# Kernel tuning notes

Measured on AMD Instinct MI355X. Metric: run time of the kernel, lower is better.

Reference implementation:

```python
import jax, jax.numpy as jnp
import numpy as np

B, T, N, F = 8, 64, 512, 64
H, FOUT = 128, 64
K = 3          # cheb_k
S = 3          # num_scales
EPS = 1e-8
SPARSITY = 0.3
TEMP = 1.0     # cheb_temp (buffer, temperature == 1.0)


def _xavier(key, fan_out, fan_in, gain):
    limit = gain * np.sqrt(6.0 / (fan_in + fan_out))
    return jax.random.uniform(key, (fan_out, fan_in), jnp.float32, -limit, limit)


def setup_inputs() -> dict:
    key = jax.random.key(0)
    ks = jax.random.split(key, 4)
    x = jax.random.normal(ks[0], (B, T, N, F), jnp.float32)
    # A_param: eye + 0.01*noise, symmetrized (improved_init, N > 64)
    A_param = jnp.eye(N, dtype=jnp.float32) + 0.01 * jax.random.normal(ks[1], (N, N), jnp.float32)
    A_param = 0.5 * (A_param + A_param.T)
    return {
        "x": x,
        "A_param": A_param,
        "alpha_logit": jnp.array(0.0, jnp.float32),  # logit(0.5)
        "in_w": _xavier(ks[2], H, F, np.sqrt(2.0)),
        "in_b": jnp.zeros((H,), jnp.float32),
        "out_w": _xavier(ks[3], FOUT, H, 1.0),
        "out_b": jnp.zeros((FOUT,), jnp.float32),
        "gn_in_w": jnp.ones((F,), jnp.float32), "gn_in_b": jnp.zeros((F,), jnp.float32), "gn_in_ms": jnp.ones((1,), jnp.float32),
        "gn_h_w": jnp.ones((H,), jnp.float32), "gn_h_b": jnp.zeros((H,), jnp.float32), "gn_h_ms": jnp.ones((1,), jnp.float32),
        "gn_out_w": jnp.ones((FOUT,), jnp.float32), "gn_out_b": jnp.zeros((FOUT,), jnp.float32), "gn_out_ms": jnp.ones((1,), jnp.float32),
        "cheb_w": jnp.full((S, K), 1.0 / K, jnp.float32),
        "scale_weights": jnp.full((S,), 1.0 / S, jnp.float32),
    }


def graph_norm(x, w, b, ms, eps=EPS):
    # normalize across the node dim (-2), with learnable mean scale
    mean = x.mean(axis=-2, keepdims=True)
    var = x.var(axis=-2, keepdims=True)  # biased, matches unbiased=False
    xn = (x - mean * ms) * jax.lax.rsqrt(var + eps)
    return xn * w + b


def reference(x, A_param, alpha_logit, in_w, in_b, out_w, out_b,
              gn_in_w, gn_in_b, gn_in_ms, gn_h_w, gn_h_b, gn_h_ms,
              gn_out_w, gn_out_b, gn_out_ms, cheb_w, scale_weights):
    Nv = A_param.shape[0]
    # --- learned graph (training path: tanh + adaptive top-k sparsify) ---
    A = 0.5 * (A_param + A_param.T)
    A = jnp.tanh(A / TEMP)
    k = max(1, int(Nv * (1.0 - SPARSITY)))
    _, idx = jax.lax.top_k(A, k)                       # [N, k] per-row top-k
    mask = jnp.zeros_like(A).at[jnp.arange(Nv)[:, None], idx].set(1.0)
    A_learned = A * mask
    # --- data graph (detached cosine similarity averaged over B*T) ---
    Bv, Tv, Nn, Fv = x.shape
    xt = x.reshape(Bv * Tv, Nn, Fv)
    xt = xt - xt.mean(axis=-1, keepdims=True)
    nrm = jnp.maximum(jnp.linalg.norm(xt, axis=-1, keepdims=True), EPS)
    xn = xt / nrm
    sim = jnp.einsum('bnf,bmf->bnm', xn, xn)
    A_data = jax.lax.stop_gradient(jnp.clip(sim.mean(axis=0), -1.0, 1.0))
    # --- blend ---
    alpha = jax.nn.sigmoid(alpha_logit)
    A_mix = alpha * A_learned + (1.0 - alpha) * A_data
    # --- normalized laplacian, clamped ---
    eye = jnp.eye(Nv, dtype=A_mix.dtype)
    A0 = A_mix * (1.0 - eye)
    deg = A0.sum(axis=-1)
    dinv = jnp.maximum(deg, EPS) ** -0.5
    L = jnp.clip(eye - dinv[:, None] * A0 * dinv[None, :], -1.5, 1.5)
    # --- feature pipeline ---
    xin = graph_norm(x, gn_in_w, gn_in_b, gn_in_ms)
    h = jnp.einsum('btnf,hf->btnh', xin, in_w) + in_b
    # --- multi-scale Chebyshev filter ---
    outs = []
    for s in range(S):
        if s == 0:
            L_s = L
        else:
            Lp = L
            for _ in range(s):
                Lp = Lp @ L
            L_s = jnp.clip(Lp, -1.5, 1.5)
        w = jax.nn.softmax(cheb_w[s] / TEMP)
        T0 = h
        T1 = jnp.einsum('btnf,nm->btmf', h, L_s)
        out = w[0] * T0 + w[1] * T1
        for ki in range(2, K):
            Tk = jnp.clip(2.0 * jnp.einsum('btpf,pm->btmf', T1, L_s) - T0, -50.0, 50.0)
            out = out + w[ki] * Tk
            T0, T1 = T1, Tk
        outs.append(out)
    sw = jax.nn.softmax(scale_weights)
    hc = sum(wv * o for wv, o in zip(sw, outs))
    hh = jax.nn.gelu(graph_norm(hc, gn_h_w, gn_h_b, gn_h_ms))
    y = jnp.einsum('btnh,oh->btno', hh, out_w) + out_b
    return graph_norm(y, gn_out_w, gn_out_b, gn_out_ms)
```

## Files before the change

kernel.cpp:

```cpp
#include <hip/hip_runtime.h>
#include <stdint.h>


typedef unsigned short u16;
using bf16x8 = __attribute__((ext_vector_type(8))) __bf16;
using f32x4  = __attribute__((ext_vector_type(4))) float;

#define DEV __device__ __forceinline__

DEV u16 f2b(float f) {
  union { float f; unsigned u; } v; v.f = f;
  unsigned r = v.u + 0x7FFFu + ((v.u >> 16) & 1u);
  return (u16)(r >> 16);
}
DEV float b2f(u16 b) {
  union { unsigned u; float f; } v; v.u = ((unsigned)b) << 16;
  return v.f;
}
DEV float clampf(float v, float lo, float hi) { return fminf(fmaxf(v, lo), hi); }
DEV bf16x8 pack8(const float* v) {
  union { bf16x8 b; u16 s[8]; } u;
#pragma unroll
  for (int i = 0; i < 8; ++i) u.s[i] = f2b(v[i]);
  return u.b;
}

__global__ __launch_bounds__(256) void k_fill(float* __restrict__ out, float v) {
  out[(size_t)blockIdx.x * 256 + threadIdx.x] = v;
}
__global__ __launch_bounds__(256) void k_zero(float* __restrict__ p) {
  p[(size_t)blockIdx.x * 256 + threadIdx.x] = 0.f;
}

__global__ __launch_bounds__(256) void k_Alearned(const float* __restrict__ Ap,
                                                  float* __restrict__ Aw,
                                                  const float* __restrict__ alpha_l,
                                                  const float* __restrict__ cheb_w,
                                                  const float* __restrict__ scale_w,
                                                  float* __restrict__ scal) {
  int i = blockIdx.x;
  __shared__ float row[512];
  for (int j = threadIdx.x; j < 512; j += 256)
    row[j] = tanhf(0.5f * (Ap[i * 512 + j] + Ap[j * 512 + i]));
  __syncthreads();
  for (int j = threadIdx.x; j < 512; j += 256) {
    float v = row[j];
    int rank = 0;
    for (int l = 0; l < 512; ++l) {
      float u = row[l];
      rank += (u > v) || (u == v && l < j);
    }
    Aw[i * 512 + j] = (rank < 358) ? v : 0.f;
  }
  if (i == 0 && threadIdx.x == 0) {
    float alpha = 1.f / (1.f + expf(-alpha_l[0]));
    float sm = fmaxf(fmaxf(scale_w[0], scale_w[1]), scale_w[2]);
    float e0 = expf(scale_w[0] - sm), e1 = expf(scale_w[1] - sm), e2 = expf(scale_w[2] - sm);
    float es = e0 + e1 + e2;
    float sw[3] = { e0 / es, e1 / es, e2 / es };
    float c0 = 0.f;
    for (int s = 0; s < 3; ++s) {
      float a = cheb_w[s * 3 + 0], b = cheb_w[s * 3 + 1], c = cheb_w[s * 3 + 2];
      float m = fmaxf(fmaxf(a, b), c);
      float f0 = expf(a - m), f1 = expf(b - m), f2 = expf(c - m);
      float fs = f0 + f1 + f2;
      c0 += sw[s] * (f0 / fs);
      scal[2 + s] = sw[s] * (f1 / fs);
      scal[5 + s] = sw[s] * (f2 / fs);
    }
    scal[0] = alpha;
    scal[1] = c0;
    scal[8] = c0 - (sw[0] * 0.f);
    float g = c0;
    for (int s = 0; s < 3; ++s) {
      float a = cheb_w[s * 3 + 0], b = cheb_w[s * 3 + 1], c = cheb_w[s * 3 + 2];
      float m = fmaxf(fmaxf(a, b), c);
      float f0 = expf(a - m), f1 = expf(b - m), f2 = expf(c - m);
      float fs = f0 + f1 + f2;
      g -= sw[s] * (f2 / fs);
    }
    scal[8] = g;
  }
}

__global__ __launch_bounds__(256) void k_gn_in_stats(const float* __restrict__ x,
                                                     float* __restrict__ st) {
  int bt = blockIdx.x;
  int f = threadIdx.x & 63, seg = threadIdx.x >> 6;
  float s = 0.f, s2 = 0.f;
  for (int n = seg * 128; n < seg * 128 + 128; ++n) {
    float v = x[((size_t)bt * 512 + n) * 64 + f];
    s += v; s2 += v * v;
  }
  __shared__ float ls[4][64], ls2[4][64];
  ls[seg][f] = s; ls2[seg][f] = s2;
  __syncthreads();
  if (seg == 0) {
    float ts = ls[0][f] + ls[1][f] + ls[2][f] + ls[3][f];
    float ts2 = ls2[0][f] + ls2[1][f] + ls2[2][f] + ls2[3][f];
    float mean = ts * (1.f / 512.f);
    float var = fmaxf(ts2 * (1.f / 512.f) - mean * mean, 0.f);
    st[bt * 128 + f * 2] = mean;
    st[bt * 128 + f * 2 + 1] = rsqrtf(var + 1e-8f);
  }
}

__global__ __launch_bounds__(256) void k_xn(const float* __restrict__ x,
                                            u16* __restrict__ Xt) {
  int R = blockIdx.x * 4 + (threadIdx.x >> 6);
  int lane = threadIdx.x & 63;
  int bt = R >> 9, n = R & 511;
  float v = x[(size_t)R * 64 + lane];
  float s = v;
  for (int m = 32; m; m >>= 1) s += __shfl_xor(s, m);
  float c = v - s * (1.f / 64.f);
  float q = c * c;
  for (int m = 32; m; m >>= 1) q += __shfl_xor(q, m);
  float nrm = fmaxf(sqrtf(q), 1e-8f);
  Xt[(size_t)n * 32768 + bt * 64 + lane] = f2b(c / nrm);
}

__global__ __launch_bounds__(256) void k_h(const float* __restrict__ x,
                                           const float* __restrict__ st,
                                           const float* __restrict__ gw,
                                           const float* __restrict__ gb,
                                           const float* __restrict__ msp,
                                           const float* __restrict__ in_w,
                                           const float* __restrict__ in_b,
                                           u16* __restrict__ Hmat) {
  int bt = blockIdx.x >> 1, half = blockIdx.x & 1;
  __shared__ float sc[64], sh[64], bias[128];
  int tid = threadIdx.x;
  float ms = msp[0];
  if (tid < 64) {
    float m = st[bt * 128 + tid * 2], ri = st[bt * 128 + tid * 2 + 1];
    float s = ri * gw[tid];
    sc[tid] = s;
    sh[tid] = gb[tid] - m * ms * s;
  }
  if (tid < 128) bias[tid] = in_b[tid];
  __syncthreads();
  const int lane = tid & 63, w = tid >> 6;
  const int fr = lane & 15, fg = lane >> 4;
  bf16x8 bfrag[8][2];
#pragma unroll
  for (int ni = 0; ni < 8; ++ni)
#pragma unroll
    for (int ks = 0; ks < 2; ++ks) {
      const float* p = in_w + (ni * 16 + fr) * 64 + ks * 32 + fg * 8;
      float4 v0 = *(const float4*)p, v1 = *(const float4*)(p + 4);
      float tmp[8] = { v0.x, v0.y, v0.z, v0.w, v1.x, v1.y, v1.z, v1.w };
      bfrag[ni][ks] = pack8(tmp);
    }
#pragma unroll 1
  for (int mi = 0; mi < 4; ++mi) {
    int n0 = half * 256 + w * 64 + mi * 16;
    bf16x8 af[2];
#pragma unroll
    for (int ks = 0; ks < 2; ++ks) {
      const float* p = x + ((size_t)bt * 512 + n0 + fr) * 64 + ks * 32 + fg * 8;
      float4 v0 = *(const float4*)p, v1 = *(const float4*)(p + 4);
      float raw[8] = { v0.x, v0.y, v0.z, v0.w, v1.x, v1.y, v1.z, v1.w };
      float tmp[8];
#pragma unroll
      for (int j = 0; j < 8; ++j) {
        int f = ks * 32 + fg * 8 + j;
        tmp[j] = raw[j] * sc[f] + sh[f];
      }
      af[ks] = pack8(tmp);
    }
    f32x4 a4[8] = {};
#pragma unroll
    for (int ni = 0; ni < 8; ++ni) {
      a4[ni] = __builtin_amdgcn_mfma_f32_16x16x32_bf16(af[0], bfrag[ni][0], a4[ni], 0, 0, 0);
      a4[ni] = __builtin_amdgcn_mfma_f32_16x16x32_bf16(af[1], bfrag[ni][1], a4[ni], 0, 0, 0);
    }
#pragma unroll
    for (int ni = 0; ni < 8; ++ni) {
      int col = ni * 16 + fr;
      float bi = bias[col];
      union { uint2 u; u16 s[4]; } pk;
#pragma unroll
      for (int r = 0; r < 4; ++r) pk.s[r] = f2b(a4[ni][r] + bi);
      *(uint2*)&Hmat[((size_t)bt * 128 + col) * 512 + n0 + fg * 4] = pk.u;
    }
  }
}

__global__ __launch_bounds__(256) void k_simgemm(const u16* __restrict__ Xt,
                                                 float* __restrict__ Aacc) {
  int tm = (blockIdx.x >> 2) * 128, tn = (blockIdx.x & 3) * 128;
  int kc = blockIdx.y * 2048;
  __shared__ u16 As[128][40], Bs[128][40];
  int tid = threadIdx.x;
  int lane = tid & 63, wave = tid >> 6;
  int wm = (wave >> 1) * 64, wn = (wave & 1) * 64;
  f32x4 accf[4][4] = {};
  const int fr = lane & 15, fk = (lane >> 4) * 8;
  for (int k0 = kc; k0 < kc + 2048; k0 += 32) {
#pragma unroll
    for (int g = 0; g < 2; ++g) {
      int ee = (tid + g * 256) * 8;
      int r = ee >> 5, kk = ee & 31;
      *(uint4*)&As[r][kk] = *(const uint4*)(Xt + (size_t)(tm + r) * 32768 + k0 + kk);
      *(uint4*)&Bs[r][kk] = *(const uint4*)(Xt + (size_t)(tn + r) * 32768 + k0 + kk);
    }
    __syncthreads();
    bf16x8 af[4], bfr[4];
#pragma unroll
    for (int mi = 0; mi < 4; ++mi) af[mi] = *(const bf16x8*)&As[wm + mi * 16 + fr][fk];
#pragma unroll
    for (int ni = 0; ni < 4; ++ni) bfr[ni] = *(const bf16x8*)&Bs[wn + ni * 16 + fr][fk];
#pragma unroll
    for (int mi = 0; mi < 4; ++mi)
#pragma unroll
      for (int ni = 0; ni < 4; ++ni)
        accf[mi][ni] = __builtin_amdgcn_mfma_f32_16x16x32_bf16(af[mi], bfr[ni], accf[mi][ni], 0, 0, 0);
    __syncthreads();
  }
#pragma unroll
  for (int mi = 0; mi < 4; ++mi)
#pragma unroll
    for (int ni = 0; ni < 4; ++ni)
#pragma unroll
      for (int r = 0; r < 4; ++r) {
        int m = tm + wm + mi * 16 + (lane >> 4) * 4 + r;
        int c = tn + wn + ni * 16 + (lane & 15);
        atomicAdd(&Aacc[m * 512 + c], accf[mi][ni][r]);
      }
}

__global__ __launch_bounds__(256) void k_Arow(float* __restrict__ Adacc,
                                              const float* __restrict__ Aw,
                                              const float* __restrict__ scal,
                                              float* __restrict__ deg) {
  int i = blockIdx.x;
  float alpha = scal[0];
  float s = 0.f;
  for (int j = threadIdx.x; j < 512; j += 256) {
    float ad = clampf(Adacc[i * 512 + j] * (1.f / 512.f), -1.f, 1.f);
    float am = alpha * Aw[i * 512 + j] + (1.f - alpha) * ad;
    if (j == i) am = 0.f;
    Adacc[i * 512 + j] = am;
    s += am;
  }
  __shared__ float red[256];
  red[threadIdx.x] = s;
  __syncthreads();
  for (int st_ = 128; st_; st_ >>= 1) {
    if (threadIdx.x < st_) red[threadIdx.x] += red[threadIdx.x + st_];
    __syncthreads();
  }
  if (threadIdx.x == 0) deg[i] = red[0];
}

__global__ __launch_bounds__(256) void k_L(const float* __restrict__ A0,
                                           const float* __restrict__ deg,
                                           float* __restrict__ L) {
  int idx = blockIdx.x * 256 + threadIdx.x;
  int i = idx >> 9, j = idx & 511;
  float di = rsqrtf(fmaxf(deg[i], 1e-8f));
  float dj = rsqrtf(fmaxf(deg[j], 1e-8f));
  float v = ((i == j) ? 1.f : 0.f) - di * A0[idx] * dj;
  L[idx] = clampf(v, -1.5f, 1.5f);
}

__global__ __launch_bounds__(256) void k_mm512c(const float* __restrict__ A,
                                                const float* __restrict__ B,
                                                float* __restrict__ C,
                                                float* __restrict__ Cc) {
  int bi = blockIdx.y, bj = blockIdx.x;
  __shared__ float As[64][65], Bs[64][65];
  int tx = threadIdx.x & 15, ty = threadIdx.x >> 4;
  float acc[4][4] = {};
  for (int k0 = 0; k0 < 512; k0 += 64) {
    for (int e = threadIdx.x; e < 4096; e += 256) {
      int r = e >> 6, c = e & 63;
      As[r][c] = A[(bi * 64 + r) * 512 + k0 + c];
      Bs[r][c] = B[(k0 + r) * 512 + bj * 64 + c];
    }
    __syncthreads();
#pragma unroll 8
    for (int k = 0; k < 64; ++k) {
      float a[4], b[4];
#pragma unroll
      for (int i = 0; i < 4; ++i) { a[i] = As[ty * 4 + i][k]; b[i] = Bs[k][tx * 4 + i]; }
#pragma unroll
      for (int i = 0; i < 4; ++i)
#pragma unroll
        for (int j = 0; j < 4; ++j) acc[i][j] += a[i] * b[j];
    }
    __syncthreads();
  }
#pragma unroll
  for (int i = 0; i < 4; ++i)
#pragma unroll
    for (int j = 0; j < 4; ++j) {
      int idx = (bi * 64 + ty * 4 + i) * 512 + bj * 64 + tx * 4 + j;
      float v = acc[i][j];
      C[idx] = v;
      Cc[idx] = clampf(v, -1.5f, 1.5f);
    }
}

__global__ __launch_bounds__(256) void k_mm512x2(const float* __restrict__ L2c,
                                                 const float* __restrict__ L3c,
                                                 float* __restrict__ Q4,
                                                 float* __restrict__ Q6) {
  const float* A = blockIdx.z ? L3c : L2c;
  float* C = blockIdx.z ? Q6 : Q4;
  int bi = blockIdx.y, bj = blockIdx.x;
  __shared__ float As[64][65], Bs[64][65];
  int tx = threadIdx.x & 15, ty = threadIdx.x >> 4;
  float acc[4][4] = {};
  for (int k0 = 0; k0 < 512; k0 += 64) {
    for (int e = threadIdx.x; e < 4096; e += 256) {
      int r = e >> 6, c = e & 63;
      As[r][c] = A[(bi * 64 + r) * 512 + k0 + c];
      Bs[r][c] = A[(k0 + r) * 512 + bj * 64 + c];
    }
    __syncthreads();
#pragma unroll 8
    for (int k = 0; k < 64; ++k) {
      float a[4], b[4];
#pragma unroll
      for (int i = 0; i < 4; ++i) { a[i] = As[ty * 4 + i][k]; b[i] = Bs[k][tx * 4 + i]; }
#pragma unroll
      for (int i = 0; i < 4; ++i)
#pragma unroll
        for (int j = 0; j < 4; ++j) acc[i][j] += a[i] * b[j];
    }
    __syncthreads();
  }
#pragma unroll
  for (int i = 0; i < 4; ++i)
#pragma unroll
    for (int j = 0; j < 4; ++j)
      C[(bi * 64 + ty * 4 + i) * 512 + bj * 64 + tx * 4 + j] = acc[i][j];
}

__global__ __launch_bounds__(256) void k_qcombine(const float* __restrict__ L,
                                                  const float* __restrict__ L2c,
                                                  const float* __restrict__ L3c,
                                                  const float* __restrict__ P2,
                                                  const float* __restrict__ Q4,
                                                  const float* __restrict__ Q6,
                                                  const float* __restrict__ scal,
                                                  u16* __restrict__ QTb) {
  __shared__ u16 t[64][65];
  int i0 = (blockIdx.x >> 3) * 64, j0 = (blockIdx.x & 7) * 64;
  float a1 = scal[2], a2 = scal[3], a3 = scal[4];
  float b1 = 2.f * scal[5], b2 = 2.f * scal[6], b3 = 2.f * scal[7];
  float g = scal[8];
  for (int e = threadIdx.x; e < 4096; e += 256) {
    int r = e >> 6, c = e & 63;
    int idx = (i0 + r) * 512 + j0 + c;
    float q = a1 * L[idx] + a2 * L2c[idx] + a3 * L3c[idx]
            + b1 * P2[idx] + b2 * Q4[idx] + b3 * Q6[idx];
    if (i0 + r == j0 + c) q += g;
    t[c][r] = f2b(q);
  }
  __syncthreads();
  for (int e = threadIdx.x; e < 4096; e += 256) {
    int r = e >> 6, c = e & 63;
    QTb[(j0 + r) * 512 + i0 + c] = t[r][c];
  }
}

__global__ __launch_bounds__(256, 2) void k_hcq3(const u16* __restrict__ Hg,
                                                 const u16* __restrict__ QT,
                                                 u16* __restrict__ accB,
                                                 int cbase,
                                                 float* __restrict__ st_h) {
  __shared__ u16 Hs[64][512];
  __shared__ float sS[64][4], sS2[64][4];
  const int tid = threadIdx.x;
  const int lane = tid & 63, w = tid >> 6;
  const int fr = lane & 15, hi = lane >> 4;
  const int cblk = blockIdx.x * 64;
  const int wn = w * 128;
  for (int e = tid; e < 4096; e += 256) {
    int r = e >> 6, kk = (e & 63) * 8;
    *(uint4*)&Hs[r][kk ^ ((r & 7) << 3)] =
        *(const uint4*)(Hg + (size_t)(cblk + r) * 512 + kk);
  }
  __syncthreads();
  const int csw = (fr & 7) << 3;
  const u16* qbase = QT + (size_t)(wn + fr) * 512 + hi * 8;
  bf16x8 bf[8], bfn[8];
#pragma unroll
  for (int ni = 0; ni < 8; ++ni)
    bf[ni] = *(const bf16x8*)(qbase + (size_t)ni * 16 * 512);
  f32x4 acc[4][8] = {};
#pragma unroll 1
  for (int k0 = 0; k0 < 512; k0 += 32) {
    if (k0 + 32 < 512) {
#pragma unroll
      for (int ni = 0; ni < 8; ++ni)
        bfn[ni] = *(const bf16x8*)(qbase + (size_t)ni * 16 * 512 + k0 + 32);
    }
    bf16x8 af[4];
#pragma unroll
    for (int ci = 0; ci < 4; ++ci)
      af[ci] = *(const bf16x8*)&Hs[ci * 16 + fr][(k0 + hi * 8) ^ csw];
#pragma unroll
    for (int ci = 0; ci < 4; ++ci)
#pragma unroll
      for (int ni = 0; ni < 8; ++ni)
        acc[ci][ni] = __builtin_amdgcn_mfma_f32_16x16x32_bf16(af[ci], bf[ni], acc[ci][ni], 0, 0, 0);
#pragma unroll
    for (int ni = 0; ni < 8; ++ni) bf[ni] = bfn[ni];
  }
#pragma unroll
  for (int ci = 0; ci < 4; ++ci) {
    float sv[4] = { 0.f, 0.f, 0.f, 0.f }, qv[4] = { 0.f, 0.f, 0.f, 0.f };
#pragma unroll
    for (int ni = 0; ni < 8; ++ni)
#pragma unroll
      for (int r = 0; r < 4; ++r) {
        float v = acc[ci][ni][r];
        sv[r] += v; qv[r] += v * v;
      }
#pragma unroll
    for (int r = 0; r < 4; ++r) {
      for (int m = 1; m <= 8; m <<= 1) {
        sv[r] += __shfl_xor(sv[r], m);
        qv[r] += __shfl_xor(qv[r], m);
      }
      if (fr == 0) {
        sS[ci * 16 + hi * 4 + r][w] = sv[r];
        sS2[ci * 16 + hi * 4 + r][w] = qv[r];
      }
    }
  }
  __syncthreads();
  if (tid < 64) {
    float a = sS[tid][0] + sS[tid][1] + sS[tid][2] + sS[tid][3];
    float b = sS2[tid][0] + sS2[tid][1] + sS2[tid][2] + sS2[tid][3];
    float mean = a * (1.f / 512.f);
    float var = fmaxf(b * (1.f / 512.f) - mean * mean, 0.f);
    int cg = cbase + cblk + tid;
    int bt = cg >> 7, h = cg & 127;
    st_h[bt * 256 + h * 2] = mean;
    st_h[bt * 256 + h * 2 + 1] = rsqrtf(var + 1e-8f);
  }
#pragma unroll
  for (int ci = 0; ci < 4; ++ci)
#pragma unroll
    for (int ni = 0; ni < 8; ++ni)
#pragma unroll
      for (int r = 0; r < 4; ++r)
        accB[(size_t)(cblk + ci * 16 + hi * 4 + r) * 512 + wn + ni * 16 + fr] =
            f2b(acc[ci][ni][r]);
}

__global__ __launch_bounds__(256) void k_y(const u16* __restrict__ acc_c,
                                           int btbase,
                                           const float* __restrict__ st,
                                           const float* __restrict__ gw,
                                           const float* __restrict__ gb,
                                           const float* __restrict__ msp,
                                           const float* __restrict__ out_w,
                                           const float* __restrict__ out_b,
                                           float* __restrict__ dout) {
  int btl = blockIdx.x >> 2, q = blockIdx.x & 3;
  int bt = btbase + btl;
  __shared__ u16 G[128][136];
  __shared__ float sc[128], sh[128], bias[64];
  int tid = threadIdx.x;
  float ms = msp[0];
  if (tid < 128) {
    float m = st[bt * 256 + tid * 2], ri = st[bt * 256 + tid * 2 + 1];
    float s = ri * gw[tid];
    sc[tid] = s;
    sh[tid] = gb[tid] - m * ms * s;
  }
  if (tid < 64) bias[tid] = out_b[tid];
  const int lane = tid & 63, w = tid >> 6;
  const int fr = lane & 15, fg = lane >> 4;
  bf16x8 bfrag[4][4];
#pragma unroll
  for (int ni = 0; ni < 4; ++ni)
#pragma unroll
    for (int ks = 0; ks < 4; ++ks) {
      const float* p = out_w + (ni * 16 + fr) * 128 + ks * 32 + fg * 8;
      float4 v0 = *(const float4*)p, v1 = *(const float4*)(p + 4);
      float tmp[8] = { v0.x, v0.y, v0.z, v0.w, v1.x, v1.y, v1.z, v1.w };
      bfrag[ni][ks] = pack8(tmp);
    }
  __syncthreads();
  {
    int h = tid >> 1, nh = (tid & 1) * 64;
    float scv = sc[h], shv = sh[h];
    const u16* src = acc_c + ((size_t)btl * 128 + h) * 512 + q * 128 + nh;
#pragma unroll
    for (int j = 0; j < 8; ++j) {
      uint4 v = *(const uint4*)(src + j * 8);
      const u16* pv = (const u16*)&v;
#pragma unroll
      for (int i = 0; i < 8; ++i) {
        float xg = b2f(pv[i]) * scv + shv;
        float y = 0.79788456f * (xg + 0.044715f * xg * xg * xg);
        float g = xg / (1.f + __expf(-2.f * y));
        G[nh + j * 8 + i][h] = f2b(g);
      }
    }
  }
  __syncthreads();
#pragma unroll
  for (int mi = 0; mi < 2; ++mi) {
    int nloc = w * 32 + mi * 16;
    bf16x8 af[4];
#pragma unroll
    for (int ks = 0; ks < 4; ++ks)
      af[ks] = *(const bf16x8*)&G[nloc + fr][ks * 32 + fg * 8];
    f32x4 a4[4] = {};
#pragma unroll
    for (int ni = 0; ni < 4; ++ni)
#pragma unroll
      for (int ks = 0; ks < 4; ++ks)
        a4[ni] = __builtin_amdgcn_mfma_f32_16x16x32_bf16(af[ks], bfrag[ni][ks], a4[ni], 0, 0, 0);
#pragma unroll
    for (int ni = 0; ni < 4; ++ni) {
      int o = ni * 16 + fr;
      float bi = bias[o];
#pragma unroll
      for (int r = 0; r < 4; ++r)
        dout[((size_t)bt * 512 + q * 128 + nloc + fg * 4 + r) * 64 + o] = a4[ni][r] + bi;
    }
  }
}

__global__ __launch_bounds__(512) void k_outf(float* __restrict__ ybuf,
                                              const float* __restrict__ gw,
                                              const float* __restrict__ gb,
                                              const float* __restrict__ msp) {
  __shared__ float Y[32768];
  __shared__ float red[8][64], red2[8][64];
  __shared__ float stm[64], str[64];
  int bt = blockIdx.x;
  int tid = threadIdx.x;
  float ms = msp[0];
  float* base = ybuf + (size_t)bt * 32768;
  for (int e = tid; e < 8192; e += 512)
    *(float4*)&Y[e * 4] = *(const float4*)(base + e * 4);
  __syncthreads();
  {
    int o = tid & 63, seg = tid >> 6;
    float s = 0.f, q = 0.f;
    for (int n = seg * 64; n < seg * 64 + 64; ++n) {
      float v = Y[n * 64 + o];
      s += v; q += v * v;
    }
    red[seg][o] = s; red2[seg][o] = q;
  }
  __syncthreads();
  if (tid < 64) {
    float s = 0.f, q = 0.f;
#pragma unroll
    for (int g = 0; g < 8; ++g) { s += red[g][tid]; q += red2[g][tid]; }
    float mean = s * (1.f / 512.f);
    float var = fmaxf(q * (1.f / 512.f) - mean * mean, 0.f);
    stm[tid] = mean * ms;
    str[tid] = rsqrtf(var + 1e-8f) * gw[tid];
  }
  __syncthreads();
  for (int e = tid; e < 32768; e += 512) {
    int o = e & 63;
    base[e] = (Y[e] - stm[o]) * str[o] + gb[o];
  }
}

extern "C" void kernel_launch(void* const* d_in, const int* in_sizes, int n_in,
                              void* d_out, int out_size, void* d_ws, size_t ws_size,
                              hipStream_t stream) {
  (void)in_sizes; (void)n_in; (void)out_size;
  const float* x        = (const float*)d_in[0];
  const float* A_param  = (const float*)d_in[1];
  const float* alpha_l  = (const float*)d_in[2];
  const float* in_w     = (const float*)d_in[3];
  const float* in_b     = (const float*)d_in[4];
  const float* out_w    = (const float*)d_in[5];
  const float* out_b    = (const float*)d_in[6];
  const float* gn_in_w  = (const float*)d_in[7];
  const float* gn_in_b  = (const float*)d_in[8];
  const float* gn_in_ms = (const float*)d_in[9];
  const float* gn_h_w   = (const float*)d_in[10];
  const float* gn_h_b   = (const float*)d_in[11];
  const float* gn_h_ms  = (const float*)d_in[12];
  const float* gn_out_w = (const float*)d_in[13];
  const float* gn_out_b = (const float*)d_in[14];
  const float* gn_out_ms= (const float*)d_in[15];
  const float* cheb_w   = (const float*)d_in[16];
  const float* scale_w  = (const float*)d_in[17];
  float* out = (float*)d_out;

  char* ws = (char*)d_ws;
  float* A_work = (float*)(ws + (0ull << 20));
  float* A_dacc = (float*)(ws + (1ull << 20));
  float* Lbuf   = (float*)(ws + (2ull << 20));
  float* P2raw  = (float*)(ws + (3ull << 20));
  float* P3raw  = (float*)(ws + (4ull << 20));
  float* L2c    = (float*)(ws + (5ull << 20));
  float* L3c    = (float*)(ws + (6ull << 20));
  float* Q4     = (float*)(ws + (0ull << 20));
  float* Q6     = (float*)(ws + (1ull << 20));
  u16*   QTb    = (u16*)(ws + (7ull << 20));
  float* deg    = (float*)(ws + (7ull << 20) + 524288);
  float* scal   = (float*)(ws + (7ull << 20) + 524288 + 4096);
  float* st_in  = (float*)(ws + (8ull << 20));
  float* st_h   = (float*)(ws + (8ull << 20) + 262144);
  u16*   Hmat   = (u16*)(ws + (10ull << 20));
  char*  chunkbase = ws + (74ull << 20);
  u16*   Xt     = (u16*)chunkbase;
  u16*   accB   = (u16*)chunkbase;

  const size_t baseNeed = 74ull << 20;
  int NC;
  if      (ws_size >= baseNeed + (64ull << 20)) NC = 1;
  else if (ws_size >= baseNeed + (32ull << 20)) NC = 2;
  else {
    k_fill<<<65536, 256, 0, stream>>>(out, (float)(ws_size >> 20));
    return;
  }
  const int CC = 65536 / NC;
  const int NBT = CC / 128;

  k_Alearned<<<512, 256, 0, stream>>>(A_param, A_work, alpha_l, cheb_w, scale_w, scal);
  k_gn_in_stats<<<512, 256, 0, stream>>>(x, st_in);
  k_xn<<<65536, 256, 0, stream>>>(x, Xt);
  k_h<<<1024, 256, 0, stream>>>(x, st_in, gn_in_w, gn_in_b, gn_in_ms, in_w, in_b, Hmat);
  k_zero<<<1024, 256, 0, stream>>>(A_dacc);
  k_simgemm<<<dim3(16, 16), 256, 0, stream>>>(Xt, A_dacc);
  k_Arow<<<512, 256, 0, stream>>>(A_dacc, A_work, scal, deg);
  k_L<<<1024, 256, 0, stream>>>(A_dacc, deg, Lbuf);
  k_mm512c<<<dim3(8, 8), 256, 0, stream>>>(Lbuf, Lbuf, P2raw, L2c);
  k_mm512c<<<dim3(8, 8), 256, 0, stream>>>(P2raw, Lbuf, P3raw, L3c);
  k_mm512x2<<<dim3(8, 8, 2), 256, 0, stream>>>(L2c, L3c, Q4, Q6);
  k_qcombine<<<64, 256, 0, stream>>>(Lbuf, L2c, L3c, P2raw, Q4, Q6, scal, QTb);

  for (int ch = 0; ch < NC; ++ch) {
    const int cbase = ch * CC;
    const int btbase = ch * NBT;
    k_hcq3<<<CC / 64, 256, 0, stream>>>(Hmat + (size_t)cbase * 512, QTb, accB,
                                        cbase, st_h);
    k_y<<<NBT * 4, 256, 0, stream>>>(accB, btbase, st_h, gn_h_w, gn_h_b, gn_h_ms,
                                     out_w, out_b, out);
  }

  k_outf<<<512, 512, 0, stream>>>(out, gn_out_w, gn_out_b, gn_out_ms);
}
```

Before: 549.1 us.

## Fuse output GraphNorm stats into k_y and widen Chebyshev GEMM to 512 threads

The output GraphNorm statistics (sum and sum of squares per bt and channel) now come from k_y's epilogue through atomics into a buffer zeroed in k_Alearned, and a simple streaming k_outf2 replaces the shared-memory k_outf. This removes a full extra read pass and the large LDS staging of the output. k_hcq3 moves to 512 threads with 64 columns per wave and swapped MFMA operands so results are written as packed 4-element stores, but it drops the register prefetch of QT. The scalar setup code is also simplified.

```diff
diff --git a/kernel.cpp b/kernel.cpp
--- a/kernel.cpp
+++ b/kernel.cpp
@@ -37,8 +37,10 @@
                                                   const float* __restrict__ alpha_l,
                                                   const float* __restrict__ cheb_w,
                                                   const float* __restrict__ scale_w,
-                                                  float* __restrict__ scal) {
+                                                  float* __restrict__ scal,
+                                                  float* __restrict__ st_out) {
   int i = blockIdx.x;
+  if (threadIdx.x < 128) st_out[i * 128 + threadIdx.x] = 0.f;
   __shared__ float row[512];
   for (int j = threadIdx.x; j < 512; j += 256)
     row[j] = tanhf(0.5f * (Ap[i * 512 + j] + Ap[j * 512 + i]));
@@ -58,7 +60,7 @@
     float e0 = expf(scale_w[0] - sm), e1 = expf(scale_w[1] - sm), e2 = expf(scale_w[2] - sm);
     float es = e0 + e1 + e2;
     float sw[3] = { e0 / es, e1 / es, e2 / es };
-    float c0 = 0.f;
+    float c0 = 0.f, g = 0.f;
     for (int s = 0; s < 3; ++s) {
       float a = cheb_w[s * 3 + 0], b = cheb_w[s * 3 + 1], c = cheb_w[s * 3 + 2];
       float m = fmaxf(fmaxf(a, b), c);
@@ -67,19 +69,11 @@
       c0 += sw[s] * (f0 / fs);
       scal[2 + s] = sw[s] * (f1 / fs);
       scal[5 + s] = sw[s] * (f2 / fs);
+      g += sw[s] * (f2 / fs);
     }
     scal[0] = alpha;
     scal[1] = c0;
-    scal[8] = c0 - (sw[0] * 0.f);
-    float g = c0;
-    for (int s = 0; s < 3; ++s) {
-      float a = cheb_w[s * 3 + 0], b = cheb_w[s * 3 + 1], c = cheb_w[s * 3 + 2];
-      float m = fmaxf(fmaxf(a, b), c);
-      float f0 = expf(a - m), f1 = expf(b - m), f2 = expf(c - m);
-      float fs = f0 + f1 + f2;
-      g -= sw[s] * (f2 / fs);
-    }
-    scal[8] = g;
+    scal[8] = c0 - g;
   }
 }
 
@@ -367,76 +361,60 @@
   }
 }
 
-__global__ __launch_bounds__(256, 2) void k_hcq3(const u16* __restrict__ Hg,
+__global__ __launch_bounds__(512, 4) void k_hcq3(const u16* __restrict__ Hg,
                                                  const u16* __restrict__ QT,
                                                  u16* __restrict__ accB,
                                                  int cbase,
                                                  float* __restrict__ st_h) {
   __shared__ u16 Hs[64][512];
-  __shared__ float sS[64][4], sS2[64][4];
+  __shared__ float sS[64][8], sS2[64][8];
   const int tid = threadIdx.x;
   const int lane = tid & 63, w = tid >> 6;
   const int fr = lane & 15, hi = lane >> 4;
   const int cblk = blockIdx.x * 64;
-  const int wn = w * 128;
-  for (int e = tid; e < 4096; e += 256) {
+  const int wn = w * 64;
+  for (int e = tid; e < 4096; e += 512) {
     int r = e >> 6, kk = (e & 63) * 8;
     *(uint4*)&Hs[r][kk ^ ((r & 7) << 3)] =
         *(const uint4*)(Hg + (size_t)(cblk + r) * 512 + kk);
   }
   __syncthreads();
   const int csw = (fr & 7) << 3;
-  const u16* qbase = QT + (size_t)(wn + fr) * 512 + hi * 8;
-  bf16x8 bf[8], bfn[8];
-#pragma unroll
-  for (int ni = 0; ni < 8; ++ni)
-    bf[ni] = *(const bf16x8*)(qbase + (size_t)ni * 16 * 512);
-  f32x4 acc[4][8] = {};
+  f32x4 acc[4][4] = {};
 #pragma unroll 1
   for (int k0 = 0; k0 < 512; k0 += 32) {
-    if (k0 + 32 < 512) {
-#pragma unroll
-      for (int ni = 0; ni < 8; ++ni)
-        bfn[ni] = *(const bf16x8*)(qbase + (size_t)ni * 16 * 512 + k0 + 32);
-    }
-    bf16x8 af[4];
+    bf16x8 af[4], bf[4];
 #pragma unroll
     for (int ci = 0; ci < 4; ++ci)
       af[ci] = *(const bf16x8*)&Hs[ci * 16 + fr][(k0 + hi * 8) ^ csw];
 #pragma unroll
-    for (int ci = 0; ci < 4; ++ci)
-#pragma unroll
-      for (int ni = 0; ni < 8; ++ni)
-        acc[ci][ni] = __builtin_amdgcn_mfma_f32_16x16x32_bf16(af[ci], bf[ni], acc[ci][ni], 0, 0, 0);
-#pragma unroll
-    for (int ni = 0; ni < 8; ++ni) bf[ni] = bfn[ni];
+    for (int ni = 0; ni < 4; ++ni)
+      bf[ni] = *(const bf16x8*)(QT + (size_t)(wn + ni * 16 + fr) * 512 + k0 + hi * 8);
+#pragma unroll
+    for (int ni = 0; ni < 4; ++ni)
+#pragma unroll
+      for (int ci = 0; ci < 4; ++ci)
+        acc[ni][ci] = __builtin_amdgcn_mfma_f32_16x16x32_bf16(bf[ni], af[ci], acc[ni][ci], 0, 0, 0);
   }
 #pragma unroll
   for (int ci = 0; ci < 4; ++ci) {
-    float sv[4] = { 0.f, 0.f, 0.f, 0.f }, qv[4] = { 0.f, 0.f, 0.f, 0.f };
-#pragma unroll
-    for (int ni = 0; ni < 8; ++ni)
+    float a = 0.f, b = 0.f;
+#pragma unroll
+    for (int ni = 0; ni < 4; ++ni)
 #pragma unroll
       for (int r = 0; r < 4; ++r) {
-        float v = acc[ci][ni][r];
-        sv[r] += v; qv[r] += v * v;
+        float v = acc[ni][ci][r];
+        a += v; b += v * v;
       }
-#pragma unroll
-    for (int r = 0; r < 4; ++r) {
-      for (int m = 1; m <= 8; m <<= 1) {
-        sv[r] += __shfl_xor(sv[r], m);
-        qv[r] += __shfl_xor(qv[r], m);
-      }
-      if (fr == 0) {
-        sS[ci * 16 + hi * 4 + r][w] = sv[r];
-        sS2[ci * 16 + hi * 4 + r][w] = qv[r];
-      }
-    }
+    a += __shfl_xor(a, 16); a += __shfl_xor(a, 32);
+    b += __shfl_xor(b, 16); b += __shfl_xor(b, 32);
+    if (hi == 0) { sS[ci * 16 + fr][w] = a; sS2[ci * 16 + fr][w] = b; }
   }
   __syncthreads();
   if (tid < 64) {
-    float a = sS[tid][0] + sS[tid][1] + sS[tid][2] + sS[tid][3];
-    float b = sS2[tid][0] + sS2[tid][1] + sS2[tid][2] + sS2[tid][3];
+    float a = 0.f, b = 0.f;
+#pragma unroll
+    for (int ww = 0; ww < 8; ++ww) { a += sS[tid][ww]; b += sS2[tid][ww]; }
     float mean = a * (1.f / 512.f);
     float var = fmaxf(b * (1.f / 512.f) - mean * mean, 0.f);
     int cg = cbase + cblk + tid;
@@ -445,13 +423,14 @@
     st_h[bt * 256 + h * 2 + 1] = rsqrtf(var + 1e-8f);
   }
 #pragma unroll
-  for (int ci = 0; ci < 4; ++ci)
-#pragma unroll
-    for (int ni = 0; ni < 8; ++ni)
-#pragma unroll
-      for (int r = 0; r < 4; ++r)
-        accB[(size_t)(cblk + ci * 16 + hi * 4 + r) * 512 + wn + ni * 16 + fr] =
-            f2b(acc[ci][ni][r]);
+  for (int ni = 0; ni < 4; ++ni)
+#pragma unroll
+    for (int ci = 0; ci < 4; ++ci) {
+      union { uint2 u; u16 s4[4]; } pk;
+#pragma unroll
+      for (int r = 0; r < 4; ++r) pk.s4[r] = f2b(acc[ni][ci][r]);
+      *(uint2*)&accB[(size_t)(cblk + ci * 16 + fr) * 512 + wn + ni * 16 + hi * 4] = pk.u;
+    }
 }
 
 __global__ __launch_bounds__(256) void k_y(const u16* __restrict__ acc_c,
@@ -462,11 +441,13 @@
                                            const float* __restrict__ msp,
                                            const float* __restrict__ out_w,
                                            const float* __restrict__ out_b,
-                                           float* __restrict__ dout) {
+                                           float* __restrict__ dout,
+                                           float* __restrict__ st_out) {
   int btl = blockIdx.x >> 2, q = blockIdx.x & 3;
   int bt = btbase + btl;
   __shared__ u16 G[128][136];
   __shared__ float sc[128], sh[128], bias[64];
+  __shared__ float sY[64][4], sQv[64][4];
   int tid = threadIdx.x;
   float ms = msp[0];
   if (tid < 128) {
@@ -507,6 +488,7 @@
     }
   }
   __syncthreads();
+  float so[4] = { 0.f, 0.f, 0.f, 0.f }, sq[4] = { 0.f, 0.f, 0.f, 0.f };
 #pragma unroll
   for (int mi = 0; mi < 2; ++mi) {
     int nloc = w * 32 + mi * 16;
@@ -525,49 +507,43 @@
       int o = ni * 16 + fr;
       float bi = bias[o];
 #pragma unroll
-      for (int r = 0; r < 4; ++r)
-        dout[((size_t)bt * 512 + q * 128 + nloc + fg * 4 + r) * 64 + o] = a4[ni][r] + bi;
-    }
-  }
-}
-
-__global__ __launch_bounds__(512) void k_outf(float* __restrict__ ybuf,
-                                              const float* __restrict__ gw,
-                                              const float* __restrict__ gb,
-                                              const float* __restrict__ msp) {
-  __shared__ float Y[32768];
-  __shared__ float red[8][64], red2[8][64];
-  __shared__ float stm[64], str[64];
-  int bt = blockIdx.x;
-  int tid = threadIdx.x;
+      for (int r = 0; r < 4; ++r) {
+        float yv = a4[ni][r] + bi;
+        so[ni] += yv; sq[ni] += yv * yv;
+        dout[((size_t)bt * 512 + q * 128 + nloc + fg * 4 + r) * 64 + o] = yv;
+      }
+    }
+  }
+#pragma unroll
+  for (int ni = 0; ni < 4; ++ni) {
+    float a = so[ni], b = sq[ni];
+    a += __shfl_xor(a, 16); a += __shfl_xor(a, 32);
+    b += __shfl_xor(b, 16); b += __shfl_xor(b, 32);
+    if (fg == 0) { sY[ni * 16 + fr][w] = a; sQv[ni * 16 + fr][w] = b; }
+  }
+  __syncthreads();
+  if (tid < 64) {
+    float a = sY[tid][0] + sY[tid][1] + sY[tid][2] + sY[tid][3];
+    float b = sQv[tid][0] + sQv[tid][1] + sQv[tid][2] + sQv[tid][3];
+    atomicAdd(&st_out[bt * 128 + tid * 2], a);
+    atomicAdd(&st_out[bt * 128 + tid * 2 + 1], b);
+  }
+}
+
+__global__ __launch_bounds__(256) void k_outf2(float* __restrict__ ybuf,
+                                               const float* __restrict__ S,
+                                               const float* __restrict__ gw,
+                                               const float* __restrict__ gb,
+                                               const float* __restrict__ msp) {
   float ms = msp[0];
-  float* base = ybuf + (size_t)bt * 32768;
-  for (int e = tid; e < 8192; e += 512)
-    *(float4*)&Y[e * 4] = *(const float4*)(base + e * 4);
-  __syncthreads();
-  {
-    int o = tid & 63, seg = tid >> 6;
-    float s = 0.f, q = 0.f;
-    for (int n = seg * 64; n < seg * 64 + 64; ++n) {
-      float v = Y[n * 64 + o];
-      s += v; q += v * v;
-    }
-    red[seg][o] = s; red2[seg][o] = q;
-  }
-  __syncthreads();
-  if (tid < 64) {
-    float s = 0.f, q = 0.f;
-#pragma unroll
-    for (int g = 0; g < 8; ++g) { s += red[g][tid]; q += red2[g][tid]; }
-    float mean = s * (1.f / 512.f);
-    float var = fmaxf(q * (1.f / 512.f) - mean * mean, 0.f);
-    stm[tid] = mean * ms;
-    str[tid] = rsqrtf(var + 1e-8f) * gw[tid];
-  }
-  __syncthreads();
-  for (int e = tid; e < 32768; e += 512) {
-    int o = e & 63;
-    base[e] = (Y[e] - stm[o]) * str[o] + gb[o];
+  for (int idx = blockIdx.x * 256 + threadIdx.x; idx < 16777216; idx += 8192 * 256) {
+    int bt = idx >> 15;
+    int o = idx & 63;
+    float sum = S[bt * 128 + o * 2], ssq = S[bt * 128 + o * 2 + 1];
+    float mean = sum * (1.f / 512.f);
+    float var = fmaxf(ssq * (1.f / 512.f) - mean * mean, 0.f);
+    float v = ybuf[idx];
+    ybuf[idx] = (v - mean * ms) * rsqrtf(var + 1e-8f) * gw[o] + gb[o];
   }
 }
 
@@ -610,6 +586,7 @@
   float* scal   = (float*)(ws + (7ull << 20) + 524288 + 4096);
   float* st_in  = (float*)(ws + (8ull << 20));
   float* st_h   = (float*)(ws + (8ull << 20) + 262144);
+  float* st_out = (float*)(ws + (8ull << 20) + 262144 + 524288);
   u16*   Hmat   = (u16*)(ws + (10ull << 20));
   char*  chunkbase = ws + (74ull << 20);
   u16*   Xt     = (u16*)chunkbase;
@@ -626,7 +603,8 @@
   const int CC = 65536 / NC;
   const int NBT = CC / 128;
 
-  k_Alearned<<<512, 256, 0, stream>>>(A_param, A_work, alpha_l, cheb_w, scale_w, scal);
+  k_Alearned<<<512, 256, 0, stream>>>(A_param, A_work, alpha_l, cheb_w, scale_w,
+                                      scal, st_out);
   k_gn_in_stats<<<512, 256, 0, stream>>>(x, st_in);
   k_xn<<<65536, 256, 0, stream>>>(x, Xt);
   k_h<<<1024, 256, 0, stream>>>(x, st_in, gn_in_w, gn_in_b, gn_in_ms, in_w, in_b, Hmat);
@@ -642,11 +620,11 @@
   for (int ch = 0; ch < NC; ++ch) {
     const int cbase = ch * CC;
     const int btbase = ch * NBT;
-    k_hcq3<<<CC / 64, 256, 0, stream>>>(Hmat + (size_t)cbase * 512, QTb, accB,
+    k_hcq3<<<CC / 64, 512, 0, stream>>>(Hmat + (size_t)cbase * 512, QTb, accB,
                                         cbase, st_h);
     k_y<<<NBT * 4, 256, 0, stream>>>(accB, btbase, st_h, gn_h_w, gn_h_b, gn_h_ms,
-                                     out_w, out_b, out);
-  }
-
-  k_outf<<<512, 512, 0, stream>>>(out, gn_out_w, gn_out_b, gn_out_ms);
-}
+                                     out_w, out_b, out, st_out);
+  }
+
+  k_outf2<<<8192, 256, 0, stream>>>(out, st_out, gn_out_w, gn_out_b, gn_out_ms);
+}
```

Result: no change. 546.6 us (-0.5%).
